# Kernel tuning notes

Measured on AMD Instinct MI355X. Metric: run time of the kernel, lower is better.

Reference implementation:

```python
import jax, jax.numpy as jnp
import numpy as np

OUT_H = 7
OUT_W = 7
RATIO = 2  # sampling_ratio (static)


def _roi_align(feat, boxes, out_h, out_w, sx, sy, ratio):
    """torchvision-style RoIAlign (aligned=False) on a single image.
    feat: [C,H,W], boxes: [N,4] (x1,y1,x2,y2) in image coords.
    sx, sy: spatial scales (W_feat/W_img, H_feat/H_img). Returns [N,C,out_h,out_w]."""
    C, H, W = feat.shape
    N = boxes.shape[0]
    x1 = boxes[:, 0] * sx
    y1 = boxes[:, 1] * sy
    x2 = boxes[:, 2] * sx
    y2 = boxes[:, 3] * sy
    rw = jnp.maximum(x2 - x1, 1.0)
    rh = jnp.maximum(y2 - y1, 1.0)
    bw = rw / out_w
    bh = rh / out_h
    offs = (jnp.arange(ratio, dtype=feat.dtype) + 0.5) / ratio  # sub-bin sample offsets
    # sample coordinates: [N, out*ratio]
    gy = y1[:, None, None] + (jnp.arange(out_h, dtype=feat.dtype)[None, :, None] + offs[None, None, :]) * bh[:, None, None]
    gx = x1[:, None, None] + (jnp.arange(out_w, dtype=feat.dtype)[None, :, None] + offs[None, None, :]) * bw[:, None, None]
    Y = gy.reshape(N, out_h * ratio)
    X = gx.reshape(N, out_w * ratio)
    vy = (Y >= -1.0) & (Y <= H)
    vx = (X >= -1.0) & (X <= W)
    Yc = jnp.clip(Y, 0.0, H - 1)
    Xc = jnp.clip(X, 0.0, W - 1)
    y0 = jnp.floor(Yc).astype(jnp.int32)
    x0 = jnp.floor(Xc).astype(jnp.int32)
    y1i = jnp.minimum(y0 + 1, H - 1)
    x1i = jnp.minimum(x0 + 1, W - 1)
    ly = Yc - y0.astype(Yc.dtype)
    lx = Xc - x0.astype(Xc.dtype)
    hy = 1.0 - ly
    hx = 1.0 - lx

    def g(yi, xi):  # corner gather -> [C, N, out_h*ratio, out_w*ratio]
        return feat[:, yi[:, :, None], xi[:, None, :]]

    val = (hy[:, :, None] * hx[:, None, :]) * g(y0, x0) \
        + (hy[:, :, None] * lx[:, None, :]) * g(y0, x1i) \
        + (ly[:, :, None] * hx[:, None, :]) * g(y1i, x0) \
        + (ly[:, :, None] * lx[:, None, :]) * g(y1i, x1i)
    valid = vy[:, :, None] & vx[:, None, :]
    val = jnp.where(valid[None], val, 0.0)
    # average over the ratio x ratio sampling grid (always divide by ratio^2)
    val = val.reshape(C, N, out_h, ratio, out_w, ratio).mean(axis=(3, 5))
    return val.transpose(1, 0, 2, 3)


def setup_inputs() -> dict:
    key = jax.random.key(0)
    k0, k1, k2, kb = jax.random.split(key, 4)
    img_h, img_w = 800, 1216
    feat0 = jax.random.normal(k0, (1, 256, 200, 304), dtype=jnp.float32)
    feat1 = jax.random.normal(k1, (1, 256, 100, 152), dtype=jnp.float32)
    feat2 = jax.random.normal(k2, (1, 256, 50, 76), dtype=jnp.float32)
    u = jax.random.uniform(kb, (256, 4), dtype=jnp.float32)
    bx1 = u[:, 0] * (img_w - 32)
    by1 = u[:, 1] * (img_h - 32)
    bw = 16.0 + u[:, 2] * 256.0
    bh = 16.0 + u[:, 3] * 256.0
    bx2 = jnp.minimum(bx1 + bw, float(img_w))
    by2 = jnp.minimum(by1 + bh, float(img_h))
    boxes = jnp.stack([bx1, by1, bx2, by2], axis=1)
    return {"feat0": feat0, "feat1": feat1, "feat2": feat2, "boxes": boxes,
            "img_h": img_h, "img_w": img_w}


def reference(feat0, feat1, feat2, boxes, img_h, img_w):
    _, C, H, W = feat0.shape
    # upsample coarser levels by 2**i, half-pixel bilinear == torch align_corners=False
    ups = [feat0]
    for i, f in enumerate([feat1, feat2], 1):
        s = 2 ** i
        ups.append(jax.image.resize(
            f, (f.shape[0], f.shape[1], f.shape[2] * s, f.shape[3] * s), method='bilinear'))
    fused = jnp.concatenate(ups, axis=1)[0]  # [3C, H, W] (single image)
    sx = W / img_w
    sy = H / img_h
    return _roi_align(fused, boxes, OUT_H, OUT_W, sx, sy, RATIO)
```

## Files before the change

kernel.cpp:

```cpp
#include <hip/hip_runtime.h>
#include <hip/hip_fp16.h>

#define H0 200
#define W0 304
#define H1 100
#define W1 152
#define H2 50
#define W2 76
#define CPL 256
#define CTOT 768
#define OH 7
#define OW 7
#define NPOS 49
#define SROW2 772

#define P0 (H0*W0)
#define P1 (H1*W1)
#define P2 (H2*W2)
#define T0_OFF ((size_t)0)
#define T1_OFF ((size_t)P0*CPL)
#define T2_OFF ((size_t)P0*CPL + (size_t)P1*CPL)
#define WS_ELEMS ((size_t)P0*CPL + (size_t)P1*CPL + (size_t)P2*CPL)
#define WS_BYTES (WS_ELEMS * 2)

__device__ __forceinline__ float hat01(float d) {
    return fmaxf(0.0f, 1.0f - fabsf(d));
}

__device__ __forceinline__ unsigned short f2h_rne(float x) {
    return __half_as_ushort(__float2half_rn(x));
}

__global__ void __launch_bounds__(256)
transpose_all_kernel(const float* __restrict__ f0, const float* __restrict__ f1,
                     const float* __restrict__ f2,
                     unsigned short* __restrict__ T0,
                     unsigned short* __restrict__ T1,
                     unsigned short* __restrict__ T2, int n0, int n01) {
    __shared__ unsigned short tile[64][72];
    int b = blockIdx.x;
    const float* in; unsigned short* outp; int P; int rel;
    if (b < n0)       { in = f0; outp = T0; P = P0; rel = b; }
    else if (b < n01) { in = f1; outp = T1; P = P1; rel = b - n0; }
    else              { in = f2; outp = T2; P = P2; rel = b - n01; }
    int p0 = (rel >> 2) * 64;
    int c0 = (rel & 3) * 64;

    int q = threadIdx.x & 15;
    int r = threadIdx.x >> 4;
    bool full = (p0 + 64 <= P);
#pragma unroll
    for (int i = 0; i < 4; ++i) {
        int c = c0 + r + 16 * i;
        int p = p0 + 4 * q;
        float4 v;
        if (full) {
            v = *(const float4*)(in + (size_t)c * P + p);
        } else {
            v.x = (p + 0 < P) ? in[(size_t)c * P + p + 0] : 0.0f;
            v.y = (p + 1 < P) ? in[(size_t)c * P + p + 1] : 0.0f;
            v.z = (p + 2 < P) ? in[(size_t)c * P + p + 2] : 0.0f;
            v.w = (p + 3 < P) ? in[(size_t)c * P + p + 3] : 0.0f;
        }
        tile[4 * q + 0][r + 16 * i] = f2h_rne(v.x);
        tile[4 * q + 1][r + 16 * i] = f2h_rne(v.y);
        tile[4 * q + 2][r + 16 * i] = f2h_rne(v.z);
        tile[4 * q + 3][r + 16 * i] = f2h_rne(v.w);
    }
    __syncthreads();
    int q8 = threadIdx.x & 7;
    int r8 = threadIdx.x >> 3;
#pragma unroll
    for (int i = 0; i < 2; ++i) {
        int p = p0 + r8 + 32 * i;
        if (p < P) {
            uint4 w = *(const uint4*)&tile[r8 + 32 * i][8 * q8];
            *(uint4*)(outp + (size_t)p * CPL + c0 + 8 * q8) = w;
        }
    }
}

template<int TY, int TX>
__device__ __forceinline__ void proc_level(const __half* __restrict__ T,
                                           const int (*__restrict__ sidx)[6],
                                           const float (*__restrict__ sw)[6],
                                           float* __restrict__ srow,
                                           unsigned co, int ow) {
    unsigned yo[TY]; float yw[TY];
#pragma unroll
    for (int j = 0; j < TY; ++j) { yo[j] = (unsigned)sidx[0][j]; yw[j] = sw[0][j]; }
    unsigned xo[TX]; __half2 xw2[TX];
#pragma unroll
    for (int j = 0; j < TX; ++j) {
        xo[j] = (unsigned)sidx[1 + ow][j];
        xw2[j] = __float2half2_rn(sw[1 + ow][j]);
    }
    float a0 = 0.f, a1 = 0.f, a2 = 0.f, a3 = 0.f;
    float a4 = 0.f, a5 = 0.f, a6 = 0.f, a7 = 0.f;
#pragma unroll
    for (int a = 0; a < TY; ++a) {
        unsigned ro = yo[a] + co;
        __half2 r0 = __float2half2_rn(0.0f);
        __half2 r1 = r0, r2 = r0, r3 = r0;
#pragma unroll
        for (int b = 0; b < TX; ++b) {
            uint4 v = *(const uint4*)(T + (ro + xo[b]));
            r0 = __hfma2(xw2[b], *(const __half2*)&v.x, r0);
            r1 = __hfma2(xw2[b], *(const __half2*)&v.y, r1);
            r2 = __hfma2(xw2[b], *(const __half2*)&v.z, r2);
            r3 = __hfma2(xw2[b], *(const __half2*)&v.w, r3);
        }
        float wa = yw[a];
        a0 = fmaf(wa, __low2float(r0), a0);  a1 = fmaf(wa, __high2float(r0), a1);
        a2 = fmaf(wa, __low2float(r1), a2);  a3 = fmaf(wa, __high2float(r1), a3);
        a4 = fmaf(wa, __low2float(r2), a4);  a5 = fmaf(wa, __high2float(r2), a5);
        a6 = fmaf(wa, __low2float(r3), a6);  a7 = fmaf(wa, __high2float(r3), a7);
    }
    float4 o0, o1;
    o0.x = a0 * 0.25f; o0.y = a1 * 0.25f; o0.z = a2 * 0.25f; o0.w = a3 * 0.25f;
    o1.x = a4 * 0.25f; o1.y = a5 * 0.25f; o1.z = a6 * 0.25f; o1.w = a7 * 0.25f;
    *(float4*)(srow + co) = o0;
    *(float4*)(srow + co + 4) = o1;
}

__global__ void __launch_bounds__(256, 6)
roi_align_row_kernel(const unsigned short* __restrict__ T0p,
                     const unsigned short* __restrict__ T1p,
                     const unsigned short* __restrict__ T2p,
                     const float* __restrict__ boxes,
                     const int* __restrict__ img_h_p,
                     const int* __restrict__ img_w_p,
                     float* __restrict__ out) {
    __shared__ float sout[OW][SROW2];
    __shared__ int   s_idx[3][8][6];
    __shared__ float s_w[3][8][6];

    const int n = blockIdx.x;
    const int oh = blockIdx.y;
    const int tid = threadIdx.x;

    if (tid < 24) {
        int lev = tid >> 3;
        int o8 = tid & 7;
        int axis = (o8 > 0) ? 1 : 0;
        int o = axis ? (o8 - 1) : oh;
        int Hc = (lev == 0) ? H0 : (lev == 1) ? H1 : H2;
        int Wc = (lev == 0) ? W0 : (lev == 1) ? W1 : W2;
        float inv_s = (lev == 0) ? 1.0f : (lev == 1) ? 0.5f : 0.25f;
        float sx = (float)W0 / (float)img_w_p[0];
        float sy = (float)H0 / (float)img_h_p[0];
        float a1v, bs; int Hf, Hca, mul;
        if (axis) {
            a1v = boxes[n * 4 + 0] * sx;
            float a2v = boxes[n * 4 + 2] * sx;
            bs = fmaxf(a2v - a1v, 1.0f) * (1.0f / (float)OW);
            Hf = W0; Hca = Wc; mul = 1;
        } else {
            a1v = boxes[n * 4 + 1] * sy;
            float a2v = boxes[n * 4 + 3] * sy;
            bs = fmaxf(a2v - a1v, 1.0f) * (1.0f / (float)OH);
            Hf = H0; Hca = Hc; mul = Wc;
        }
        int idx[6]; float w[6];
#pragma unroll
        for (int j = 0; j < 6; ++j) { idx[j] = 0; w[j] = 0.0f; }
        if (lev == 0) {
#pragma unroll
            for (int r2 = 0; r2 < 2; ++r2) {
                float Y = a1v + ((float)o + 0.25f + 0.5f * (float)r2) * bs;
                float v = (Y >= -1.0f && Y <= (float)Hf) ? 1.0f : 0.0f;
                float Yc = fminf(fmaxf(Y, 0.0f), (float)(Hf - 1));
                int y0 = (int)Yc; float lf = Yc - (float)y0;
                idx[2 * r2]     = y0;                  w[2 * r2]     = (1.0f - lf) * v;
                idx[2 * r2 + 1] = min(y0 + 1, Hf - 1); w[2 * r2 + 1] = lf * v;
            }
        } else {
            int bases[2]; float w3[2][3];
#pragma unroll
            for (int r2 = 0; r2 < 2; ++r2) {
                float Y = a1v + ((float)o + 0.25f + 0.5f * (float)r2) * bs;
                float v = (Y >= -1.0f && Y <= (float)Hf) ? 1.0f : 0.0f;
                float Yc = fminf(fmaxf(Y, 0.0f), (float)(Hf - 1));
                int y0 = (int)Yc; float lf = Yc - (float)y0; float hf = 1.0f - lf;
                int yf1 = min(y0 + 1, Hf - 1);
                float yc0 = fminf(fmaxf(((float)y0 + 0.5f) * inv_s - 0.5f, 0.0f), (float)(Hca - 1));
                float yc1 = fminf(fmaxf(((float)yf1 + 0.5f) * inv_s - 0.5f, 0.0f), (float)(Hca - 1));
                int b2 = (int)yc0;
                bases[r2] = b2;
#pragma unroll
                for (int t2 = 0; t2 < 3; ++t2) {
                    float j2 = (float)(b2 + t2);
                    w3[r2][t2] = v * (hf * hat01(yc0 - j2) + lf * hat01(yc1 - j2));
                }
            }
            int dmax = (lev == 1) ? 3 : 2;
            int d = min(max(bases[1] - bases[0], 0), dmax);
            w[0] += w3[0][0]; w[1] += w3[0][1]; w[2] += w3[0][2];
            w[d] += w3[1][0]; w[d + 1] += w3[1][1]; w[d + 2] += w3[1][2];
#pragma unroll
            for (int j = 0; j < 6; ++j) idx[j] = min(bases[0] + j, Hca - 1);
        }
#pragma unroll
        for (int j = 0; j < 6; ++j) { s_idx[lev][o8][j] = idx[j] * mul * CPL; s_w[lev][o8][j] = w[j]; }
    }
    __syncthreads();

    const int lane = tid & 63;
    const int wv = tid >> 6;
    const int half = lane >> 5;
    const int l = lane & 31;
    int ow = 2 * wv + half;
    ow = (ow > OW - 1) ? (OW - 1) : ow;
    unsigned co = (unsigned)(l * 8);
    float* srow = &sout[ow][0];

    proc_level<4, 4>((const __half*)T0p, s_idx[0], s_w[0], srow,           co, ow);
    proc_level<6, 6>((const __half*)T1p, s_idx[1], s_w[1], srow + CPL,     co, ow);
    proc_level<5, 5>((const __half*)T2p, s_idx[2], s_w[2], srow + 2 * CPL, co, ow);
    __syncthreads();

    size_t obase = (size_t)n * CTOT * NPOS + (size_t)oh * OW;
    for (int i2 = tid; i2 < CTOT * OW; i2 += 256) {
        int c = i2 / OW;
        int p = i2 - c * OW;
        out[obase + (size_t)c * NPOS + p] = sout[p][c];
    }
}

__device__ __forceinline__ void axis_w3_fb(int yf0, int Hf, int Hc, float inv_s,
                                           float lf, int& base, float* w) {
    int yf1 = min(yf0 + 1, Hf - 1);
    float hf = 1.0f - lf;
    float yc0 = fminf(fmaxf(((float)yf0 + 0.5f) * inv_s - 0.5f, 0.0f), (float)(Hc - 1));
    float yc1 = fminf(fmaxf(((float)yf1 + 0.5f) * inv_s - 0.5f, 0.0f), (float)(Hc - 1));
    base = (int)yc0;
#pragma unroll
    for (int r = 0; r < 3; ++r) {
        float j = (float)(base + r);
        w[r] = hf * hat01(yc0 - j) + lf * hat01(yc1 - j);
    }
}

__global__ void __launch_bounds__(256)
roi_align_fused_fb_kernel(const float* __restrict__ f0,
                          const float* __restrict__ f1,
                          const float* __restrict__ f2,
                          const float* __restrict__ boxes,
                          const int* __restrict__ img_h_p,
                          const int* __restrict__ img_w_p,
                          float* __restrict__ out,
                          int total) {
    int i = blockIdx.x * blockDim.x + threadIdx.x;
    if (i >= total) return;
    int ow = i % OW;
    int t = i / OW;
    int oh = t % OH; t /= OH;
    int c = t % CTOT;
    int n = t / CTOT;
    float sx = (float)W0 / (float)img_w_p[0];
    float sy = (float)H0 / (float)img_h_p[0];
    float bx1 = boxes[n * 4 + 0] * sx;
    float by1 = boxes[n * 4 + 1] * sy;
    float bw = fmaxf(boxes[n * 4 + 2] * sx - bx1, 1.0f) / OW;
    float bh = fmaxf(boxes[n * 4 + 3] * sy - by1, 1.0f) / OH;
    int level = c >> 8;
    int cl = c & (CPL - 1);
    const float* f;
    int Hc, Wc; float inv_s;
    if (level == 0)      { f = f0 + (size_t)cl * P0; Hc = H0; Wc = W0; inv_s = 1.0f;  }
    else if (level == 1) { f = f1 + (size_t)cl * P1; Hc = H1; Wc = W1; inv_s = 0.5f;  }
    else                 { f = f2 + (size_t)cl * P2; Hc = H2; Wc = W2; inv_s = 0.25f; }
    float acc = 0.0f;
#pragma unroll
    for (int ry = 0; ry < 2; ++ry) {
        float Y = by1 + ((float)oh + 0.25f + 0.5f * ry) * bh;
        bool vy = (Y >= -1.0f) && (Y <= (float)H0);
        float Yc = fminf(fmaxf(Y, 0.0f), (float)(H0 - 1));
        int y0 = (int)Yc;
        float ly = Yc - (float)y0;
#pragma unroll
        for (int rx = 0; rx < 2; ++rx) {
            float X = bx1 + ((float)ow + 0.25f + 0.5f * rx) * bw;
            bool vx = (X >= -1.0f) && (X <= (float)W0);
            float Xc = fminf(fmaxf(X, 0.0f), (float)(W0 - 1));
            int x0 = (int)Xc;
            float lx = Xc - (float)x0;
            float v;
            if (level == 0) {
                int y1i = min(y0 + 1, H0 - 1), x1i = min(x0 + 1, W0 - 1);
                float hy = 1.0f - ly, hx = 1.0f - lx;
                float v00 = f[y0 * W0 + x0],  v01 = f[y0 * W0 + x1i];
                float v10 = f[y1i * W0 + x0], v11 = f[y1i * W0 + x1i];
                v = hy * (hx * v00 + lx * v01) + ly * (hx * v10 + lx * v11);
            } else {
                int yb, xb; float wy[3], wxl[3];
                axis_w3_fb(y0, H0, Hc, inv_s, ly, yb, wy);
                axis_w3_fb(x0, W0, Wc, inv_s, lx, xb, wxl);
                v = 0.0f;
#pragma unroll
                for (int a = 0; a < 3; ++a) {
                    int row = min(yb + a, Hc - 1) * Wc;
                    float s = 0.0f;
#pragma unroll
                    for (int b = 0; b < 3; ++b)
                        s += wxl[b] * f[row + min(xb + b, Wc - 1)];
                    v += wy[a] * s;
                }
            }
            if (vy && vx) acc += v;
        }
    }
    out[i] = acc * 0.25f;
}

extern "C" void kernel_launch(void* const* d_in, const int* in_sizes, int n_in,
                              void* d_out, int out_size, void* d_ws, size_t ws_size,
                              hipStream_t stream) {
    const float* f0    = (const float*)d_in[0];
    const float* f1    = (const float*)d_in[1];
    const float* f2    = (const float*)d_in[2];
    const float* boxes = (const float*)d_in[3];
    const int* img_h_p = (const int*)d_in[4];
    const int* img_w_p = (const int*)d_in[5];
    float* out = (float*)d_out;
    int N = in_sizes[3] / 4;

    if (ws_size >= WS_BYTES) {
        unsigned short* ws = (unsigned short*)d_ws;
        unsigned short* T0 = ws + T0_OFF;
        unsigned short* T1 = ws + T1_OFF;
        unsigned short* T2 = ws + T2_OFF;
        int n0 = ((P0 + 63) / 64) * 4;
        int n1 = ((P1 + 63) / 64) * 4;
        int n2 = ((P2 + 63) / 64) * 4;
        transpose_all_kernel<<<n0 + n1 + n2, 256, 0, stream>>>(
            f0, f1, f2, T0, T1, T2, n0, n0 + n1);
        roi_align_row_kernel<<<dim3(N, OH), 256, 0, stream>>>(
            T0, T1, T2, boxes, img_h_p, img_w_p, out);
    } else {
        int total = N * CTOT * OH * OW;
        roi_align_fused_fb_kernel<<<(total + 255) / 256, 256, 0, stream>>>(
            f0, f1, f2, boxes, img_h_p, img_w_p, out, total);
    }
}
```

Baseline: 177.7 us.

## Split RoI blocks by pyramid level and channel half instead of output row

Restructures the RoI align kernel so each block handles one pyramid level and a 128-channel half for all 49 output positions, rather than one output row across all levels. This gives contiguous coalesced output writes and a uniform tap count per block. It trades this for load imbalance between level blocks and fewer blocks in the grid.

```diff
diff --git a/kernel.cpp b/kernel.cpp
--- a/kernel.cpp
+++ b/kernel.cpp
@@ -12,7 +12,8 @@
 #define OH 7
 #define OW 7
 #define NPOS 49
-#define SROW2 772
+#define CBLK 128
+#define SROWP 131
 
 #define P0 (H0*W0)
 #define P1 (H1*W1)
@@ -81,72 +82,78 @@
 }
 
 template<int TY, int TX>
-__device__ __forceinline__ void proc_level(const __half* __restrict__ T,
-                                           const int (*__restrict__ sidx)[6],
-                                           const float (*__restrict__ sw)[6],
-                                           float* __restrict__ srow,
-                                           unsigned co, int ow) {
-    unsigned yo[TY]; float yw[TY];
-#pragma unroll
-    for (int j = 0; j < TY; ++j) { yo[j] = (unsigned)sidx[0][j]; yw[j] = sw[0][j]; }
-    unsigned xo[TX]; __half2 xw2[TX];
-#pragma unroll
-    for (int j = 0; j < TX; ++j) {
-        xo[j] = (unsigned)sidx[1 + ow][j];
-        xw2[j] = __float2half2_rn(sw[1 + ow][j]);
-    }
-    float a0 = 0.f, a1 = 0.f, a2 = 0.f, a3 = 0.f;
-    float a4 = 0.f, a5 = 0.f, a6 = 0.f, a7 = 0.f;
-#pragma unroll
-    for (int a = 0; a < TY; ++a) {
-        unsigned ro = yo[a] + co;
-        __half2 r0 = __float2half2_rn(0.0f);
-        __half2 r1 = r0, r2 = r0, r3 = r0;
-#pragma unroll
-        for (int b = 0; b < TX; ++b) {
-            uint4 v = *(const uint4*)(T + (ro + xo[b]));
-            r0 = __hfma2(xw2[b], *(const __half2*)&v.x, r0);
-            r1 = __hfma2(xw2[b], *(const __half2*)&v.y, r1);
-            r2 = __hfma2(xw2[b], *(const __half2*)&v.z, r2);
-            r3 = __hfma2(xw2[b], *(const __half2*)&v.w, r3);
-        }
-        float wa = yw[a];
-        a0 = fmaf(wa, __low2float(r0), a0);  a1 = fmaf(wa, __high2float(r0), a1);
-        a2 = fmaf(wa, __low2float(r1), a2);  a3 = fmaf(wa, __high2float(r1), a3);
-        a4 = fmaf(wa, __low2float(r2), a4);  a5 = fmaf(wa, __high2float(r2), a5);
-        a6 = fmaf(wa, __low2float(r3), a6);  a7 = fmaf(wa, __high2float(r3), a7);
-    }
-    float4 o0, o1;
-    o0.x = a0 * 0.25f; o0.y = a1 * 0.25f; o0.z = a2 * 0.25f; o0.w = a3 * 0.25f;
-    o1.x = a4 * 0.25f; o1.y = a5 * 0.25f; o1.z = a6 * 0.25f; o1.w = a7 * 0.25f;
-    *(float4*)(srow + co) = o0;
-    *(float4*)(srow + co + 4) = o1;
+__device__ __forceinline__ void tap_loop(const __half* __restrict__ Tc,
+                                         const int (*__restrict__ s_idx)[6],
+                                         const float (*__restrict__ s_w)[6],
+                                         float (*__restrict__ sout)[SROWP],
+                                         int grp, int col) {
+    for (int pos = grp; pos < NPOS; pos += 16) {
+        int oh = pos / 7;
+        int ow = pos - oh * 7;
+        unsigned yo[TY]; float yw[TY];
+#pragma unroll
+        for (int j = 0; j < TY; ++j) { yo[j] = (unsigned)s_idx[oh][j];     yw[j] = s_w[oh][j]; }
+        unsigned xo[TX]; __half2 xw2[TX];
+#pragma unroll
+        for (int j = 0; j < TX; ++j) {
+            xo[j] = (unsigned)s_idx[7 + ow][j];
+            xw2[j] = __float2half2_rn(s_w[7 + ow][j]);
+        }
+        float a0 = 0.f, a1 = 0.f, a2 = 0.f, a3 = 0.f;
+        float a4 = 0.f, a5 = 0.f, a6 = 0.f, a7 = 0.f;
+#pragma unroll
+        for (int a = 0; a < TY; ++a) {
+            unsigned ro = yo[a];
+            __half2 r0 = __float2half2_rn(0.0f);
+            __half2 r1 = r0, r2 = r0, r3 = r0;
+#pragma unroll
+            for (int b = 0; b < TX; ++b) {
+                uint4 v = *(const uint4*)(Tc + (ro + xo[b]));
+                r0 = __hfma2(xw2[b], *(const __half2*)&v.x, r0);
+                r1 = __hfma2(xw2[b], *(const __half2*)&v.y, r1);
+                r2 = __hfma2(xw2[b], *(const __half2*)&v.z, r2);
+                r3 = __hfma2(xw2[b], *(const __half2*)&v.w, r3);
+            }
+            float wa = yw[a];
+            a0 = fmaf(wa, __low2float(r0), a0);  a1 = fmaf(wa, __high2float(r0), a1);
+            a2 = fmaf(wa, __low2float(r1), a2);  a3 = fmaf(wa, __high2float(r1), a3);
+            a4 = fmaf(wa, __low2float(r2), a4);  a5 = fmaf(wa, __high2float(r2), a5);
+            a6 = fmaf(wa, __low2float(r3), a6);  a7 = fmaf(wa, __high2float(r3), a7);
+        }
+        float4 o0, o1;
+        o0.x = a0 * 0.25f; o0.y = a1 * 0.25f; o0.z = a2 * 0.25f; o0.w = a3 * 0.25f;
+        o1.x = a4 * 0.25f; o1.y = a5 * 0.25f; o1.z = a6 * 0.25f; o1.w = a7 * 0.25f;
+        *(float4*)(&sout[pos][col])     = o0;
+        *(float4*)(&sout[pos][col + 4]) = o1;
+    }
 }
 
 __global__ void __launch_bounds__(256, 6)
-roi_align_row_kernel(const unsigned short* __restrict__ T0p,
+roi_align_cl6_kernel(const unsigned short* __restrict__ T0p,
                      const unsigned short* __restrict__ T1p,
                      const unsigned short* __restrict__ T2p,
                      const float* __restrict__ boxes,
                      const int* __restrict__ img_h_p,
                      const int* __restrict__ img_w_p,
                      float* __restrict__ out) {
-    __shared__ float sout[OW][SROW2];
-    __shared__ int   s_idx[3][8][6];
-    __shared__ float s_w[3][8][6];
+    __shared__ float sout[NPOS][SROWP];
+    __shared__ int   s_idx[14][6];
+    __shared__ float s_w[14][6];
 
     const int n = blockIdx.x;
-    const int oh = blockIdx.y;
+    const int j = blockIdx.y;
+    const int lev = j >> 1;
+    const int chalf = j & 1;
     const int tid = threadIdx.x;
 
-    if (tid < 24) {
-        int lev = tid >> 3;
-        int o8 = tid & 7;
-        int axis = (o8 > 0) ? 1 : 0;
-        int o = axis ? (o8 - 1) : oh;
-        int Hc = (lev == 0) ? H0 : (lev == 1) ? H1 : H2;
-        int Wc = (lev == 0) ? W0 : (lev == 1) ? W1 : W2;
-        float inv_s = (lev == 0) ? 1.0f : (lev == 1) ? 0.5f : 0.25f;
+    const unsigned short* T; int Hc, Wc; float inv_s;
+    if (lev == 0)      { T = T0p; Hc = H0; Wc = W0; inv_s = 1.0f;  }
+    else if (lev == 1) { T = T1p; Hc = H1; Wc = W1; inv_s = 0.5f;  }
+    else               { T = T2p; Hc = H2; Wc = W2; inv_s = 0.25f; }
+
+    if (tid < 14) {
+        int axis = (tid >= 7) ? 1 : 0;
+        int o = tid - axis * 7;
         float sx = (float)W0 / (float)img_w_p[0];
         float sy = (float)H0 / (float)img_h_p[0];
         float a1v, bs; int Hf, Hca, mul;
@@ -163,7 +170,7 @@
         }
         int idx[6]; float w[6];
 #pragma unroll
-        for (int j = 0; j < 6; ++j) { idx[j] = 0; w[j] = 0.0f; }
+        for (int t = 0; t < 6; ++t) { idx[t] = 0; w[t] = 0.0f; }
         if (lev == 0) {
 #pragma unroll
             for (int r2 = 0; r2 < 2; ++r2) {
@@ -198,32 +205,30 @@
             w[0] += w3[0][0]; w[1] += w3[0][1]; w[2] += w3[0][2];
             w[d] += w3[1][0]; w[d + 1] += w3[1][1]; w[d + 2] += w3[1][2];
 #pragma unroll
-            for (int j = 0; j < 6; ++j) idx[j] = min(bases[0] + j, Hca - 1);
-        }
-#pragma unroll
-        for (int j = 0; j < 6; ++j) { s_idx[lev][o8][j] = idx[j] * mul * CPL; s_w[lev][o8][j] = w[j]; }
+            for (int t = 0; t < 6; ++t) idx[t] = min(bases[0] + t, Hca - 1);
+        }
+#pragma unroll
+        for (int t = 0; t < 6; ++t) { s_idx[tid][t] = idx[t] * mul * CPL; s_w[tid][t] = w[t]; }
     }
     __syncthreads();
 
-    const int lane = tid & 63;
-    const int wv = tid >> 6;
-    const int half = lane >> 5;
-    const int l = lane & 31;
-    int ow = 2 * wv + half;
-    ow = (ow > OW - 1) ? (OW - 1) : ow;
-    unsigned co = (unsigned)(l * 8);
-    float* srow = &sout[ow][0];
-
-    proc_level<4, 4>((const __half*)T0p, s_idx[0], s_w[0], srow,           co, ow);
-    proc_level<6, 6>((const __half*)T1p, s_idx[1], s_w[1], srow + CPL,     co, ow);
-    proc_level<5, 5>((const __half*)T2p, s_idx[2], s_w[2], srow + 2 * CPL, co, ow);
+    const int grp = tid >> 4;
+    const int l16 = tid & 15;
+    const int col = l16 * 8;
+    const __half* Tc = (const __half*)T + (chalf * CBLK + col);
+
+    if (lev == 0)      tap_loop<4, 4>(Tc, s_idx, s_w, sout, grp, col);
+    else if (lev == 1) tap_loop<6, 6>(Tc, s_idx, s_w, sout, grp, col);
+    else               tap_loop<5, 5>(Tc, s_idx, s_w, sout, grp, col);
     __syncthreads();
 
-    size_t obase = (size_t)n * CTOT * NPOS + (size_t)oh * OW;
-    for (int i2 = tid; i2 < CTOT * OW; i2 += 256) {
-        int c = i2 / OW;
-        int p = i2 - c * OW;
-        out[obase + (size_t)c * NPOS + p] = sout[p][c];
+    size_t obase = (size_t)n * CTOT * NPOS + (size_t)(lev * CPL + chalf * CBLK) * NPOS;
+    int c = tid / NPOS;
+    int p = tid - c * NPOS;
+    for (int i = tid; i < CBLK * NPOS; i += 256) {
+        out[obase + i] = sout[p][c];
+        c += 5; p += 11;
+        if (p >= NPOS) { p -= NPOS; ++c; }
     }
 }
 
@@ -335,7 +340,7 @@
         int n2 = ((P2 + 63) / 64) * 4;
         transpose_all_kernel<<<n0 + n1 + n2, 256, 0, stream>>>(
             f0, f1, f2, T0, T1, T2, n0, n0 + n1);
-        roi_align_row_kernel<<<dim3(N, OH), 256, 0, stream>>>(
+        roi_align_cl6_kernel<<<dim3(N, 6), 256, 0, stream>>>(
             T0, T1, T2, boxes, img_h_p, img_w_p, out);
     } else {
         int total = N * CTOT * OH * OW;
```

Measured after the change: 160.8 us. -9.5%, faster.
